# Kernel tuning notes

Measured on AMD Instinct MI355X. Metric: run time of the kernel, lower is better.

## Reference

```python
import jax, jax.numpy as jnp
import numpy as np

NH = 8          # attention heads
NC = 14         # disease classes
K = 10          # aspect queries per class
E = 1024        # vision_dim == text_dim
HID = 512       # hidden_dim = vision_dim // 2
TEMP = 0.1
LN_EPS = 1e-5


def _layernorm(x, g, b):
    m = jnp.mean(x, axis=-1, keepdims=True)
    v = jnp.mean(jnp.square(x - m), axis=-1, keepdims=True)
    return (x - m) * jax.lax.rsqrt(v + LN_EPS) * g + b


def _mha(q, k, v, in_w, in_b, out_w, out_b):
    # nn.MultiheadAttention (batch_first, eval mode => dropout off)
    B, Lq, Emb = q.shape
    Lk = k.shape[1]
    dh = Emb // NH
    wq, wk, wv = jnp.split(in_w, 3, axis=0)
    bq, bk, bv = jnp.split(in_b, 3)
    qh = (q @ wq.T + bq).reshape(B, Lq, NH, dh)
    kh = (k @ wk.T + bk).reshape(B, Lk, NH, dh)
    vh = (v @ wv.T + bv).reshape(B, Lk, NH, dh)
    scale = np.float32(1.0 / np.sqrt(dh))
    scores = jnp.einsum('bqhd,bkhd->bhqk', qh, kh) * scale
    attn = jax.nn.softmax(scores, axis=-1)
    out = jnp.einsum('bhqk,bkhd->bqhd', attn, vh).reshape(B, Lq, Emb)
    out = out @ out_w.T + out_b
    return out, attn.mean(axis=1)  # avg over heads, (B, Lq, Lk)


def _l2norm(x):
    return x / jnp.maximum(jnp.linalg.norm(x, axis=-1, keepdims=True), 1e-12)


def reference(vision_features, text_embeddings, vision_global, aspect_queries,
              ch_in_w, ch_in_b, ch_out_w, ch_out_b, tp_w, tp_b,
              ca_in_w, ca_in_b, ca_out_w, ca_out_b,
              cross_ln_g, cross_ln_b, cross_fc_w, cross_fc_b,
              dir_ln_g, dir_ln_b, dir_w1, dir_b1, dir_w2, dir_b2):
    B, N, _ = vision_features.shape
    # ---- contrastive branch (1-token query / 1-token kv attention) ----
    text_proj = text_embeddings @ tp_w.T + tp_b               # (B, E)
    c_out, _ = _mha(vision_global[:, None, :], text_proj[:, None, :],
                    text_proj[:, None, :], ch_in_w, ch_in_b, ch_out_w, ch_out_b)
    sim = jnp.sum(_l2norm(c_out[:, 0, :]) * _l2norm(text_proj), axis=-1) / TEMP  # (B,)
    contrastive_logits = jnp.broadcast_to(sim[:, None], (B, NC))
    # ---- supervised branch: fused per-class cross-attention (shared K/V) ----
    q = jnp.broadcast_to(aspect_queries.reshape(1, NC * K, E), (B, NC * K, E))
    att_out, attn_w = _mha(q, vision_features, vision_features,
                           ca_in_w, ca_in_b, ca_out_w, ca_out_b)
    attended = att_out.reshape(B, NC, K, E).mean(axis=2)       # (B, NC, E)
    attention_weights = attn_w.reshape(B, NC, K, N)            # (B, NC, K, N)
    # fc_cross: LN + per-class linear row (class j feature -> class j logit)
    h = _layernorm(attended, cross_ln_g, cross_ln_b)
    logits_cross = jnp.einsum('bjd,jd->bj', h, cross_fc_w) + cross_fc_b
    # fc_direct MLP on global feature
    g = _layernorm(vision_global, dir_ln_g, dir_ln_b)
    logits_direct = jax.nn.relu(g @ dir_w1.T + dir_b1) @ dir_w2.T + dir_b2
    supervised_logits = (logits_cross + logits_direct) * 0.5
    final_logits = (supervised_logits + contrastive_logits) * 0.5
    return contrastive_logits, supervised_logits, final_logits, attention_weights


def setup_inputs() -> dict:
    key = jax.random.key(0)
    ks = jax.random.split(key, 16)
    B, N = 64, 576
    w = lambda k, s: (jax.random.normal(k, s, dtype=jnp.float32) * 0.02)
    return {
        'vision_features': jax.random.normal(ks[0], (B, N, E), dtype=jnp.float32),
        'text_embeddings': jax.random.normal(ks[1], (B, E), dtype=jnp.float32),
        'vision_global': jax.random.normal(ks[2], (B, E), dtype=jnp.float32),
        'aspect_queries': jax.random.normal(ks[3], (NC, K, E), dtype=jnp.float32) / np.sqrt(E).astype(np.float32),
        'ch_in_w': w(ks[4], (3 * E, E)), 'ch_in_b': jnp.zeros((3 * E,), jnp.float32),
        'ch_out_w': w(ks[5], (E, E)), 'ch_out_b': jnp.zeros((E,), jnp.float32),
        'tp_w': w(ks[6], (E, E)), 'tp_b': jnp.zeros((E,), jnp.float32),
        'ca_in_w': w(ks[7], (3 * E, E)), 'ca_in_b': jnp.zeros((3 * E,), jnp.float32),
        'ca_out_w': w(ks[8], (E, E)), 'ca_out_b': jnp.zeros((E,), jnp.float32),
        'cross_ln_g': jnp.ones((E,), jnp.float32), 'cross_ln_b': jnp.zeros((E,), jnp.float32),
        'cross_fc_w': w(ks[9], (NC, E)), 'cross_fc_b': jnp.zeros((NC,), jnp.float32),
        'dir_ln_g': jnp.ones((E,), jnp.float32), 'dir_ln_b': jnp.zeros((E,), jnp.float32),
        'dir_w1': w(ks[10], (HID, E)), 'dir_b1': jnp.zeros((HID,), jnp.float32),
        'dir_w2': w(ks[11], (NC, HID)), 'dir_b2': jnp.zeros((NC,), jnp.float32),
    }
```

## Files before the change

kernel.cpp:

```cpp
#include <hip/hip_runtime.h>
#include <cstdio>
#include <cstdint>

using u16 = unsigned short;
typedef __bf16 bf16x8 __attribute__((ext_vector_type(8)));
typedef float f32x4 __attribute__((ext_vector_type(4)));

#define GLOBAL_AS __attribute__((address_space(1)))
#define LDS_AS __attribute__((address_space(3)))

__device__ __forceinline__ float bf2f(u16 h) {
  return __uint_as_float(((unsigned)h) << 16);
}
__device__ __forceinline__ u16 f2bf(float f) {
  unsigned u = __float_as_uint(f);
  u += 0x7FFFu + ((u >> 16) & 1u);
  return (u16)(u >> 16);
}

__device__ __forceinline__ void async_copy16(void* lds, const void* g) {
  __builtin_amdgcn_global_load_lds((const GLOBAL_AS unsigned int*)g,
                                   (LDS_AS unsigned int*)lds, 16, 0, 0);
}

__device__ __forceinline__ float block_sum(float v, float* red) {
#pragma unroll
  for (int o = 32; o >= 1; o >>= 1) v += __shfl_xor(v, o);
  __syncthreads();
  if ((threadIdx.x & 63) == 0) red[threadIdx.x >> 6] = v;
  __syncthreads();
  return red[0] + red[1] + red[2] + red[3];
}

__global__ __launch_bounds__(256) void cvt4_kernel(
    const float* __restrict__ s0, u16* __restrict__ d0,
    const float* __restrict__ s1, u16* __restrict__ d1,
    const float* __restrict__ s2, u16* __restrict__ d2,
    const float* __restrict__ s3, u16* __restrict__ d3) {
  const float* s; u16* d; long n; long b0; long nb;
  const int b = blockIdx.x;
  if (b < 2048)      { s = s0; d = d0; n = 37748736L; b0 = b;        nb = 2048; }
  else if (b < 2816) { s = s1; d = d1; n = 3145728L;  b0 = b - 2048; nb = 768; }
  else if (b < 3072) { s = s2; d = d2; n = 1048576L;  b0 = b - 2816; nb = 256; }
  else               { s = s3; d = d3; n = 143360L;   b0 = b - 3072; nb = 35; }
  long i = (b0 * 256 + threadIdx.x) * 4;
  const long stride = nb * 1024;
  for (; i < n; i += stride) {
    float4 v = *(const float4*)(s + i);
    ushort4 o;
    o.x = f2bf(v.x); o.y = f2bf(v.y); o.z = f2bf(v.z); o.w = f2bf(v.w);
    *(ushort4*)(d + i) = o;
  }
}

template <int VTD>
__global__ __launch_bounds__(512, 2) void gemm_kvq_kernel(
    const u16* __restrict__ A, const u16* __restrict__ Bkv,
    const u16* __restrict__ Aq, const u16* __restrict__ Bq,
    u16* __restrict__ Ck, u16* __restrict__ Cvp, u16* __restrict__ Vt,
    u16* __restrict__ Cq,
    const float* __restrict__ bias, const float* __restrict__ biasq) {
  __shared__ char smem[131072];
  const int bid = blockIdx.x;
  const int t = threadIdx.x;
  const int wid = t >> 6, l = t & 63;
  const int wm = wid >> 2, wn = wid & 3;
  const int lr = l & 15, lg = l >> 4, lr7 = lr & 7;

  int mt = 0, nt = 0, qb = -1;
  const u16* Abase; const u16* Bbase; const float* bias_b;
  if (bid < 1152) {
    const int wgid = (bid & 7) * 144 + (bid >> 3);
    mt = wgid >> 3; nt = wgid & 7;
    Abase = A + (size_t)mt * 256 * 1024;
    Bbase = Bkv + (size_t)nt * 256 * 1024;
    bias_b = bias + nt * 256;
  } else {
    qb = bid - 1152;
    Abase = Aq;
    Bbase = Bq + (size_t)qb * 256 * 1024;
    bias_b = biasq + qb * 256;
  }

  const int srow = t >> 3;
  const int scx = (t & 7) ^ (srow & 7);
  const char* Asrc = (const char*)Abase + (size_t)srow * 2048 + (scx << 4);
  const char* Bsrc = (const char*)Bbase + (size_t)srow * 2048 + (scx << 4);
  const int wb = wid << 10;

  f32x4 acc[8][4] = {};

#define SA(d, r, kt) async_copy16(smem + (d)*65536 + (r)*8192 + wb, \
                                  Asrc + (size_t)(r)*131072 + (size_t)(kt)*128)
#define SB(d, r, kt) async_copy16(smem + (d)*65536 + 32768 + (r)*8192 + wb, \
                                  Bsrc + (size_t)(r)*131072 + (size_t)(kt)*128)

#define RA(d, half)                                                          \
  _Pragma("unroll")                                                          \
  for (int i = 0; i < 4; ++i) {                                              \
    const int row = wm * 128 + ((half)*4 + i) * 16 + lr;                     \
    af[i][0] = *(const bf16x8*)(smem + (d)*65536 + (row << 7) + ((lg ^ lr7) << 4));       \
    af[i][1] = *(const bf16x8*)(smem + (d)*65536 + (row << 7) + (((4 | lg) ^ lr7) << 4)); \
  }

#define RB(d, half)                                                          \
  _Pragma("unroll")                                                          \
  for (int j = 0; j < 2; ++j) {                                              \
    const int row = wn * 64 + ((half)*2 + j) * 16 + lr;                      \
    bfr[j][0] = *(const bf16x8*)(smem + (d)*65536 + 32768 + (row << 7) + ((lg ^ lr7) << 4));       \
    bfr[j][1] = *(const bf16x8*)(smem + (d)*65536 + 32768 + (row << 7) + (((4 | lg) ^ lr7) << 4)); \
  }

#define MM(mh, nh)                                                           \
  __builtin_amdgcn_s_setprio(1);                                             \
  _Pragma("unroll")                                                          \
  for (int ks = 0; ks < 2; ++ks)                                             \
    _Pragma("unroll")                                                        \
    for (int i = 0; i < 4; ++i)                                              \
      _Pragma("unroll")                                                      \
      for (int j = 0; j < 2; ++j)                                            \
        acc[(mh)*4 + i][(nh)*2 + j] = __builtin_amdgcn_mfma_f32_16x16x32_bf16( \
            af[i][ks], bfr[j][ks], acc[(mh)*4 + i][(nh)*2 + j], 0, 0, 0);    \
  __builtin_amdgcn_s_setprio(0);

  SA(0, 0, 0); SA(0, 1, 0); SA(0, 2, 0); SA(0, 3, 0);
  SB(0, 0, 0); SB(0, 1, 0); SB(0, 2, 0); SB(0, 3, 0);
  SA(1, 0, 1); SA(1, 2, 1);
  asm volatile("s_waitcnt vmcnt(2)" ::: "memory");
  __builtin_amdgcn_s_barrier();
  asm volatile("" ::: "memory");

#pragma unroll 1
  for (int kt = 0; kt < 16; ++kt) {
    const int cur = kt & 1, nxt = cur ^ 1;
    const bool pf1 = (kt < 15), pf2 = (kt < 14);
    bf16x8 af[4][2], bfr[2][2];
    RA(cur, 0);
    RB(cur, 0);
    if (pf1) { SB(nxt, 0, kt + 1); SB(nxt, 1, kt + 1); }
    __builtin_amdgcn_s_barrier();
    asm volatile("s_waitcnt lgkmcnt(0)" ::: "memory");
    MM(0, 0);
    __builtin_amdgcn_s_barrier();
    RB(cur, 1);
    if (pf1) { SB(nxt, 2, kt + 1); SB(nxt, 3, kt + 1); }
    __builtin_amdgcn_s_barrier();
    asm volatile("s_waitcnt lgkmcnt(0)" ::: "memory");
    MM(0, 1);
    if (pf1) asm volatile("s_waitcnt vmcnt(6)" ::: "memory");
    __builtin_amdgcn_s_barrier();
    RA(cur, 1);
    if (pf1) { SA(nxt, 1, kt + 1); SA(nxt, 3, kt + 1); }
    __builtin_amdgcn_s_barrier();
    asm volatile("s_waitcnt lgkmcnt(0)" ::: "memory");
    MM(1, 1);
    __builtin_amdgcn_s_barrier();
    RB(cur, 0);
    if (pf2) { SA(cur, 0, kt + 2); SA(cur, 2, kt + 2); }
    __builtin_amdgcn_s_barrier();
    asm volatile("s_waitcnt lgkmcnt(0)" ::: "memory");
    MM(1, 0);
    if (pf2)      asm volatile("s_waitcnt vmcnt(4)" ::: "memory");
    else if (pf1) asm volatile("s_waitcnt vmcnt(0)" ::: "memory");
    __builtin_amdgcn_s_barrier();
  }
#undef SA
#undef SB
#undef RA
#undef RB
#undef MM

  if (VTD && qb < 0 && nt >= 4) {
    u16* T = (u16*)smem;
    const int vc2 = t >> 1, seg = t & 1;
    const int vglob = (nt - 4) * 256 + vc2;
    const int h2 = vglob >> 7, d2 = vglob & 127;
#pragma unroll 1
    for (int mh = 0; mh < 2; ++mh) {
      __syncthreads();
      if (wm == mh) {
#pragma unroll
        for (int ni = 0; ni < 4; ++ni) {
          const int vc = wn * 64 + ni * 16 + lr;
          const float bv = bias_b[vc];
#pragma unroll
          for (int mi = 0; mi < 8; ++mi) {
            const int ml = mi * 16 + lg * 4;
            ushort4 pk;
            pk.x = f2bf(acc[mi][ni][0] + bv);
            pk.y = f2bf(acc[mi][ni][1] + bv);
            pk.z = f2bf(acc[mi][ni][2] + bv);
            pk.w = f2bf(acc[mi][ni][3] + bv);
            *(ushort4*)(T + (size_t)vc * 136 + ml) = pk;
          }
        }
      }
      __syncthreads();
      const int mg0 = mt * 256 + mh * 128 + seg * 64;
      const int bb = (unsigned)mg0 / 576u;
      const int k0 = mg0 - bb * 576;
      u16* dst = Vt + ((size_t)(bb * 8 + h2) * 128 + d2) * 576 + k0;
      const u16* src = T + (size_t)vc2 * 136 + seg * 64;
#pragma unroll
      for (int i2 = 0; i2 < 8; ++i2)
        *(uint4*)(dst + i2 * 8) = *(const uint4*)(src + i2 * 8);
    }
  } else {
    u16* D; int cb0;
    if (qb >= 0)      { D = Cq;  cb0 = qb * 256; }
    else if (nt < 4)  { D = Ck;  cb0 = nt * 256; }
    else              { D = Cvp; cb0 = (nt - 4) * 256; }
#pragma unroll
    for (int ni = 0; ni < 4; ++ni) {
      const int nc = wn * 64 + ni * 16 + lr;
      const float bv = bias_b[nc];
      const int col = cb0 + nc;
#pragma unroll
      for (int mi = 0; mi < 8; ++mi) {
#pragma unroll
        for (int rg = 0; rg < 4; ++rg) {
          const size_t m = (size_t)mt * 256 + wm * 128 + mi * 16 + lg * 4 + rg;
          D[m * 1024 + col] = f2bf(acc[mi][ni][rg] + bv);
        }
      }
    }
  }
}

template <int OUTF32>
__global__ __launch_bounds__(512, 2) void gemm_big_kernel(
    const u16* __restrict__ A, const u16* __restrict__ B, void* __restrict__ Cv,
    const float* __restrict__ bias, float scale,
    int KT, int ntx, int Mlim, int Nlim,
    long lda, long ldb, long ldc, int bdiv,
    long sA0, long sA1, long sB0, long sB1, long sC0, long sC1) {
  __shared__ u16 lds[3][24576];
  const int bid = blockIdx.x;
  const int bh = blockIdx.y;
  const int bb0 = bh / bdiv, bb1 = bh % bdiv;
  const int mt = bid / ntx, nt = bid % ntx;
  const int t = threadIdx.x;
  const int wid = t >> 6, l = t & 63;
  const int wr = wid >> 1, wc = wid & 1;
  const int lr = l & 15, lg = l >> 4, lr7 = lr & 7;

  const long ldab = lda * 2, ldbb = ldb * 2;
  const u16* Abase = A + (long)bb0 * sA0 + (long)bb1 * sA1 + (long)mt * 256 * lda;
  const u16* Bbase = B + (long)bb0 * sB0 + (long)bb1 * sB1 + (long)nt * 128 * ldb;

  const int srow = t >> 3;
  const int scx = (t & 7) ^ (srow & 7);
  const char* Asrc = (const char*)Abase + (long)srow * ldab + (scx << 4);
  const char* Bsrc = (const char*)Bbase + (long)srow * ldbb + (scx << 4);
  const int wbA = wid << 10;

  char* b0 = (char*)lds[0];
  char* b1 = (char*)lds[1];
  char* b2 = (char*)lds[2];

  f32x4 acc[4][4] = {};

#define STAGE3G(dst, kt, part)                                              \
  {                                                                         \
    const long ko = (long)(kt) * 128;                                       \
    if ((part) == 0) {                                                      \
      async_copy16((dst) + wbA,          Asrc + ko);                        \
      async_copy16((dst) + 8192 + wbA,   Asrc + 64 * ldab + ko);            \
      async_copy16((dst) + 16384 + wbA,  Asrc + 128 * ldab + ko);           \
    } else {                                                                \
      async_copy16((dst) + 24576 + wbA,  Asrc + 192 * ldab + ko);           \
      async_copy16((dst) + 32768 + wbA,  Bsrc + ko);                        \
      async_copy16((dst) + 40960 + wbA,  Bsrc + 64 * ldbb + ko);            \
    }                                                                       \
  }

#define COMPUTE_KS(p, KS)                                                   \
  {                                                                         \
    const int ccol = (((KS) << 2) | lg) ^ lr7;                              \
    const char* pA = (p) + (((wr << 6) + lr) << 7) + (ccol << 4);           \
    const char* pB = (p) + 32768 + (((wc << 6) + lr) << 7) + (ccol << 4);   \
    bf16x8 af[4], bfr[4];                                                   \
    _Pragma("unroll")                                                       \
    for (int i = 0; i < 4; ++i) {                                           \
      af[i]  = *(const bf16x8*)(pA + i * 2048);                             \
      bfr[i] = *(const bf16x8*)(pB + i * 2048);                             \
    }                                                                       \
    __builtin_amdgcn_s_setprio(1);                                          \
    _Pragma("unroll")                                                       \
    for (int mi = 0; mi < 4; ++mi)                                          \
      _Pragma("unroll")                                                     \
      for (int ni = 0; ni < 4; ++ni)                                        \
        acc[mi][ni] = __builtin_amdgcn_mfma_f32_16x16x32_bf16(              \
            af[mi], bfr[ni], acc[mi][ni], 0, 0, 0);                         \
    __builtin_amdgcn_s_setprio(0);                                          \
  }

  STAGE3G(b0, 0, 0); STAGE3G(b0, 0, 1);
  STAGE3G(b1, 1, 0); STAGE3G(b1, 1, 1);
  asm volatile("s_waitcnt vmcnt(6)" ::: "memory");
  __builtin_amdgcn_s_barrier();
  asm volatile("" ::: "memory");

  char* p0 = b0; char* p1 = b1; char* p2 = b2;
#pragma unroll 1
  for (int kt = 0; kt < KT; ++kt) {
    const bool pf = (kt < KT - 2);
    if (pf) STAGE3G(p2, kt + 2, 0);
    COMPUTE_KS(p0, 0);
    if (pf) STAGE3G(p2, kt + 2, 1);
    COMPUTE_KS(p0, 1);
    if (kt < KT - 1) {
      if (pf) asm volatile("s_waitcnt vmcnt(6)" ::: "memory");
      else    asm volatile("s_waitcnt vmcnt(0)" ::: "memory");
      __builtin_amdgcn_s_barrier();
      asm volatile("" ::: "memory");
    }
    char* tmp = p0; p0 = p1; p1 = p2; p2 = tmp;
  }
#undef STAGE3G
#undef COMPUTE_KS

  const long cBase = (long)bb0 * sC0 + (long)bb1 * sC1;
  const int mr0 = mt * 256 + wr * 64 + lg * 4;
  const int nc0 = nt * 128 + wc * 64 + lr;
#pragma unroll
  for (int ni = 0; ni < 4; ++ni) {
    const int n = nc0 + ni * 16;
    if (n >= Nlim) continue;
    const float bv = bias ? bias[n] : 0.0f;
#pragma unroll
    for (int mi = 0; mi < 4; ++mi) {
#pragma unroll
      for (int rg = 0; rg < 4; ++rg) {
        const int m = mr0 + mi * 16 + rg;
        if (m >= Mlim) continue;
        const float v = acc[mi][ni][rg] * scale + bv;
        if (OUTF32) ((float*)Cv)[cBase + (long)m * ldc + n] = v;
        else        ((u16*)Cv)[cBase + (long)m * ldc + n] = f2bf(v);
      }
    }
  }
}

__global__ __launch_bounds__(256) void transpose_v_kernel(const u16* __restrict__ V,
                                                          u16* __restrict__ Vt) {
  __shared__ u16 tile[64][65];
  const int k0 = blockIdx.x * 64;
  const int c0 = blockIdx.y * 64;
  const int b = blockIdx.z;
  const int t = threadIdx.x;
  const int tx = t & 15, ty = t >> 4;
  const u16* Vb = V + (size_t)(b * 576) * 1024;
#pragma unroll
  for (int i = 0; i < 4; ++i) {
    const int k = ty + i * 16;
    const u16* src = Vb + (size_t)(k0 + k) * 1024 + c0 + tx * 4;
    ushort2 v01 = *(const ushort2*)src;
    ushort2 v23 = *(const ushort2*)(src + 2);
    tile[k][tx * 4 + 0] = v01.x; tile[k][tx * 4 + 1] = v01.y;
    tile[k][tx * 4 + 2] = v23.x; tile[k][tx * 4 + 3] = v23.y;
  }
  __syncthreads();
  const int h = c0 >> 7, d0 = c0 & 127;
  u16* VtB = Vt + ((size_t)(b * 8 + h) * 128 + d0) * 576 + k0;
#pragma unroll
  for (int i = 0; i < 4; ++i) {
    const int d = ty + i * 16;
    u16* dst = VtB + (size_t)d * 576 + tx * 4;
    ushort2 a, bb2;
    a.x = tile[tx * 4 + 0][d]; a.y = tile[tx * 4 + 1][d];
    bb2.x = tile[tx * 4 + 2][d]; bb2.y = tile[tx * 4 + 3][d];
    *(ushort2*)dst = a; *(ushort2*)(dst + 2) = bb2;
  }
}

__global__ __launch_bounds__(512) void softmax_pm_kernel(const u16* __restrict__ SP,
                                                         float* __restrict__ attnOut,
                                                         u16* __restrict__ Pm) {
  const int b = blockIdx.x, c = blockIdx.y;
  const int h = threadIdx.x >> 6, l = threadIdx.x & 63;
  __shared__ float pl[8][576];
  float pacc[9] = {};
#pragma unroll 1
  for (int qq = 0; qq < 10; ++qq) {
    const u16* row = SP + ((size_t)((b * 8 + h) * 144 + c * 10 + qq)) * 576;
    float x[9];
#pragma unroll
    for (int i = 0; i < 9; ++i) x[i] = bf2f(row[l + 64 * i]);
    float m = x[0];
#pragma unroll
    for (int i = 1; i < 9; ++i) m = fmaxf(m, x[i]);
#pragma unroll
    for (int o = 32; o >= 1; o >>= 1) m = fmaxf(m, __shfl_xor(m, o));
    float e[9], s = 0.f;
#pragma unroll
    for (int i = 0; i < 9; ++i) { e[i] = expf(x[i] - m); s += e[i]; }
#pragma unroll
    for (int o = 32; o >= 1; o >>= 1) s += __shfl_xor(s, o);
    const float inv = 1.f / s;
#pragma unroll
    for (int i = 0; i < 9; ++i) {
      const float p = e[i] * inv;
      pacc[i] += p;
      pl[h][l + 64 * i] = p;
    }
    __syncthreads();
    float* out = attnOut + ((size_t)(b * 140 + c * 10 + qq)) * 576;
    {
      const int j = threadIdx.x;
      float a = 0.f;
#pragma unroll
      for (int hh = 0; hh < 8; ++hh) a += pl[hh][j];
      out[j] = a * 0.125f;
      if (j < 64) {
        float a2 = 0.f;
#pragma unroll
        for (int hh = 0; hh < 8; ++hh) a2 += pl[hh][j + 512];
        out[j + 512] = a2 * 0.125f;
      }
    }
    __syncthreads();
  }
  u16* pm = Pm + ((size_t)((b * 8 + h) * 14 + c)) * 576;
#pragma unroll
  for (int i = 0; i < 9; ++i) pm[l + 64 * i] = f2bf(pacc[i] * 0.1f);
}

__global__ __launch_bounds__(256) void pv_small_kernel(const u16* __restrict__ Pm,
                                                       const u16* __restrict__ Vt,
                                                       u16* __restrict__ Attd) {
  const int b = blockIdx.x, h = blockIdx.y;
  const int t = threadIdx.x;
  const int w = t >> 6, l = t & 63;
  const int lr = l & 15, lg = l >> 4;
  __shared__ u16 pm[16][584];
  for (int i = t; i < 16 * 73; i += 256) {
    const int r = i / 73, ck = i - (i / 73) * 73;
    uint4 v = {0u, 0u, 0u, 0u};
    if (r < 14 && ck < 72)
      v = *(const uint4*)&Pm[((size_t)((b * 8 + h) * 14 + r)) * 576 + ck * 8];
    *(uint4*)&pm[r][ck * 8] = v;
  }
  __syncthreads();
  const u16* vbase = Vt + ((size_t)(b * 8 + h) * 128) * 576;
  f32x4 acc[2] = {};
#pragma unroll 1
  for (int ks = 0; ks < 18; ++ks) {
    const bf16x8 af = *(const bf16x8*)&pm[lr][ks * 32 + lg * 8];
#pragma unroll
    for (int j = 0; j < 2; ++j) {
      const int nf = w * 2 + j;
      const bf16x8 bf = *(const bf16x8*)&vbase[(size_t)(nf * 16 + lr) * 576 + ks * 32 + lg * 8];
      acc[j] = __builtin_amdgcn_mfma_f32_16x16x32_bf16(af, bf, acc[j], 0, 0, 0);
    }
  }
#pragma unroll
  for (int j = 0; j < 2; ++j) {
    const int nf = w * 2 + j;
#pragma unroll
    for (int rg = 0; rg < 4; ++rg) {
      const int cc = lg * 4 + rg;
      if (cc < 14)
        Attd[((size_t)b * 14 + cc) * 1024 + h * 128 + nf * 16 + lr] = f2bf(acc[j][rg]);
    }
  }
}

__global__ __launch_bounds__(256) void ln_crossfc_kernel(
    const float* __restrict__ ap, const float* __restrict__ g, const float* __restrict__ bb,
    const float* __restrict__ fw, const float* __restrict__ fb, float* __restrict__ out) {
  const int bc = blockIdx.x;
  const int c = bc % 14;
  const float* x = ap + (size_t)bc * 1024;
  __shared__ float red[4];
  const int t = threadIdx.x;
  float v[4];
  float s = 0.f;
#pragma unroll
  for (int i = 0; i < 4; ++i) { v[i] = x[t + i * 256]; s += v[i]; }
  const float mean = block_sum(s, red) * (1.f / 1024.f);
  float vs = 0.f;
#pragma unroll
  for (int i = 0; i < 4; ++i) { const float d = v[i] - mean; vs += d * d; }
  const float var = block_sum(vs, red) * (1.f / 1024.f);
  const float inv = rsqrtf(var + 1e-5f);
  float acc = 0.f;
#pragma unroll
  for (int i = 0; i < 4; ++i) {
    const int e = t + i * 256;
    const float h = (v[i] - mean) * inv * g[e] + bb[e];
    acc += h * fw[(size_t)c * 1024 + e];
  }
  acc = block_sum(acc, red);
  if (t == 0) out[bc] = acc + fb[c];
}

__global__ __launch_bounds__(256) void direct_mlp_kernel(
    const float* __restrict__ vg, const float* __restrict__ g, const float* __restrict__ bb,
    const float* __restrict__ w1, const float* __restrict__ b1,
    const float* __restrict__ w2, const float* __restrict__ b2, float* __restrict__ out) {
  const int b = blockIdx.x;
  __shared__ float red[4];
  __shared__ float gn[1024];
  __shared__ float h1[512];
  const int t = threadIdx.x;
  const float* x = vg + (size_t)b * 1024;
  float v[4];
  float s = 0.f;
#pragma unroll
  for (int i = 0; i < 4; ++i) { v[i] = x[t + i * 256]; s += v[i]; }
  const float mean = block_sum(s, red) * (1.f / 1024.f);
  float vs = 0.f;
#pragma unroll
  for (int i = 0; i < 4; ++i) { const float d = v[i] - mean; vs += d * d; }
  const float var = block_sum(vs, red) * (1.f / 1024.f);
  const float inv = rsqrtf(var + 1e-5f);
#pragma unroll
  for (int i = 0; i < 4; ++i) {
    const int e = t + i * 256;
    gn[e] = (v[i] - mean) * inv * g[e] + bb[e];
  }
  __syncthreads();
  for (int j = t; j < 512; j += 256) {
    float a = b1[j];
    const float4* wr = (const float4*)(w1 + (size_t)j * 1024);
    const float4* g4 = (const float4*)gn;
    for (int e = 0; e < 256; ++e) {
      float4 wv = wr[e], av = g4[e];
      a += av.x * wv.x + av.y * wv.y + av.z * wv.z + av.w * wv.w;
    }
    h1[j] = fmaxf(a, 0.f);
  }
  __syncthreads();
  for (int c = 0; c < 14; ++c) {
    float a = 0.f;
    for (int j = t; j < 512; j += 256) a += h1[j] * w2[(size_t)c * 512 + j];
    a = block_sum(a, red);
    if (t == 0) out[b * 14 + c] = a + b2[c];
  }
}

__global__ __launch_bounds__(256) void linear_f32_kernel(
    const float* __restrict__ A, const float* __restrict__ W, const float* __restrict__ bias,
    float* __restrict__ C, int N, int Kd) {
  const int r = blockIdx.x;
  const int j = blockIdx.y * 256 + threadIdx.x;
  __shared__ float a[1024];
  for (int e = threadIdx.x; e < Kd; e += 256) a[e] = A[(size_t)r * Kd + e];
  __syncthreads();
  float acc = bias ? bias[j] : 0.f;
  const float4* wr = (const float4*)(W + (size_t)j * Kd);
  const float4* a4 = (const float4*)a;
  for (int e = 0; e < Kd / 4; ++e) {
    float4 wv = wr[e], av = a4[e];
    acc += av.x * wv.x + av.y * wv.y + av.z * wv.z + av.w * wv.w;
  }
  C[(size_t)r * N + j] = acc;
}

__global__ __launch_bounds__(256) void sim_combine_kernel(
    const float* __restrict__ co, const float* __restrict__ tp,
    const float* __restrict__ lc, const float* __restrict__ ld,
    float* __restrict__ out) {
  const int b = blockIdx.x;
  const int t = threadIdx.x;
  __shared__ float red[4];
  const float* c = co + (size_t)b * 1024;
  const float* p = tp + (size_t)b * 1024;
  float dd = 0.f, nc = 0.f, nt = 0.f;
  for (int e = t; e < 1024; e += 256) {
    const float cv = c[e], pv = p[e];
    dd += cv * pv; nc += cv * cv; nt += pv * pv;
  }
  dd = block_sum(dd, red);
  nc = block_sum(nc, red);
  nt = block_sum(nt, red);
  const float sim = dd / (fmaxf(sqrtf(nc), 1e-12f) * fmaxf(sqrtf(nt), 1e-12f)) / 0.1f;
  if (t < 14) {
    const int i = b * 14 + t;
    const float sup = 0.5f * (lc[i] + ld[i]);
    out[i] = sim;
    out[896 + i] = sup;
    out[1792 + i] = 0.5f * (sup + sim);
  }
}

static constexpr size_t OFF_X    = 0;
static constexpr size_t OFF_K    = OFF_X + 75497472;
static constexpr size_t OFF_SP   = OFF_K + 75759616;
static constexpr size_t OFF_WIN  = OFF_SP + 85082112;
static constexpr size_t OFF_WOUT = OFF_WIN + 6291456;
static constexpr size_t OFF_ASP  = OFF_WOUT + 2097152;
static constexpr size_t OFF_QASP = OFF_ASP + 524288;
static constexpr size_t OFF_ATT  = OFF_QASP + 524288;
static constexpr size_t OFF_APRJ = OFF_ATT + 1835008;
static constexpr size_t OFF_TP   = OFF_APRJ + 3670016;
static constexpr size_t OFF_CV   = OFF_TP + 262144;
static constexpr size_t OFF_CO   = OFF_CV + 262144;
static constexpr size_t OFF_SIM  = OFF_CO + 262144;
static constexpr size_t OFF_LC   = OFF_SIM + 4096;
static constexpr size_t OFF_LD   = OFF_LC + 4096;
static constexpr size_t WS_SMALL = OFF_LD + 4096;
static constexpr size_t OFF_VT   = WS_SMALL;
static constexpr size_t WS_BIG   = OFF_VT + 75497472;

extern "C" void kernel_launch(void* const* d_in, const int* in_sizes, int n_in,
                              void* d_out, int out_size, void* d_ws, size_t ws_size,
                              hipStream_t stream) {
  (void)in_sizes; (void)n_in; (void)out_size;
  const float* vision_features = (const float*)d_in[0];
  const float* text_embeddings = (const float*)d_in[1];
  const float* vision_global   = (const float*)d_in[2];
  const float* aspect_queries  = (const float*)d_in[3];
  const float* ch_in_w  = (const float*)d_in[4];
  const float* ch_in_b  = (const float*)d_in[5];
  const float* ch_out_w = (const float*)d_in[6];
  const float* ch_out_b = (const float*)d_in[7];
  const float* tp_w = (const float*)d_in[8];
  const float* tp_b = (const float*)d_in[9];
  const float* ca_in_w  = (const float*)d_in[10];
  const float* ca_in_b  = (const float*)d_in[11];
  const float* ca_out_w = (const float*)d_in[12];
  const float* ca_out_b = (const float*)d_in[13];
  const float* cross_ln_g = (const float*)d_in[14];
  const float* cross_ln_b = (const float*)d_in[15];
  const float* cross_fc_w = (const float*)d_in[16];
  const float* cross_fc_b = (const float*)d_in[17];
  const float* dir_ln_g = (const float*)d_in[18];
  const float* dir_ln_b = (const float*)d_in[19];
  const float* dir_w1 = (const float*)d_in[20];
  const float* dir_b1 = (const float*)d_in[21];
  const float* dir_w2 = (const float*)d_in[22];
  const float* dir_b2 = (const float*)d_in[23];

  if (ws_size < WS_SMALL) {
    fprintf(stderr, "kernel_launch: ws too small: %zu < %zu\n", ws_size, WS_SMALL);
    return;
  }
  const bool big = (ws_size >= WS_BIG);

  char* ws = (char*)d_ws;
  u16* Xb      = (u16*)(ws + OFF_X);
  u16* Kb      = (u16*)(ws + OFF_K);
  u16* Pm      = (u16*)(ws + OFF_K);
  u16* Vb      = (u16*)(ws + OFF_SP);
  u16* SP      = (u16*)(ws + OFF_SP);
  u16* Vt      = big ? (u16*)(ws + OFF_VT) : (u16*)(ws + OFF_X);
  u16* Win     = (u16*)(ws + OFF_WIN);
  u16* Wout    = (u16*)(ws + OFF_WOUT);
  u16* Asp     = (u16*)(ws + OFF_ASP);
  u16* Qasp    = (u16*)(ws + OFF_QASP);
  u16* Attd    = (u16*)(ws + OFF_ATT);
  float* Aprj  = (float*)(ws + OFF_APRJ);
  float* Tp    = (float*)(ws + OFF_TP);
  float* Cv2   = (float*)(ws + OFF_CV);
  float* Co    = (float*)(ws + OFF_CO);
  float* Lc    = (float*)(ws + OFF_LC);
  float* Ld    = (float*)(ws + OFF_LD);
  float* attnOut = (float*)d_out + 2688;

  cvt4_kernel<<<3107, 256, 0, stream>>>(vision_features, Xb, ca_in_w, Win,
                                        ca_out_w, Wout, aspect_queries, Asp);

  if (big) {
    gemm_kvq_kernel<1><<<dim3(1156), 512, 0, stream>>>(
        Xb, Win + 1024 * 1024, Asp, Win, Kb, nullptr, Vt, Qasp,
        ca_in_b + 1024, ca_in_b);
  } else {
    gemm_kvq_kernel<0><<<dim3(1156), 512, 0, stream>>>(
        Xb, Win + 1024 * 1024, Asp, Win, Kb, Vb, nullptr, Qasp,
        ca_in_b + 1024, ca_in_b);
    transpose_v_kernel<<<dim3(9, 16, 64), 256, 0, stream>>>(Vb, Vt);
  }

  gemm_big_kernel<0><<<dim3(5, 512), 512, 0, stream>>>(
      Qasp, Kb, SP, nullptr, 0.08838834764831845f,
      2, 5, 140, 576, 1024, 1024, 576, 8,
      0L, 128L, 589824L, 128L, 663552L, 82944L);

  softmax_pm_kernel<<<dim3(64, 14), 512, 0, stream>>>(SP, attnOut, Pm);

  pv_small_kernel<<<dim3(64, 8), 256, 0, stream>>>(Pm, Vt, Attd);

  gemm_big_kernel<1><<<dim3(32, 1), 512, 0, stream>>>(
      Attd, Wout, Aprj, ca_out_b, 1.0f,
      16, 8, 896, 1024, 1024, 1024, 1024, 1,
      0L, 0L, 0L, 0L, 0L, 0L);

  ln_crossfc_kernel<<<896, 256, 0, stream>>>(Aprj, cross_ln_g, cross_ln_b,
                                             cross_fc_w, cross_fc_b, Lc);

  direct_mlp_kernel<<<64, 256, 0, stream>>>(vision_global, dir_ln_g, dir_ln_b,
                                            dir_w1, dir_b1, dir_w2, dir_b2, Ld);

  linear_f32_kernel<<<dim3(64, 4), 256, 0, stream>>>(text_embeddings, tp_w, tp_b, Tp, 1024, 1024);
  linear_f32_kernel<<<dim3(64, 4), 256, 0, stream>>>(Tp, ch_in_w + 2048 * 1024, ch_in_b + 2048, Cv2, 1024, 1024);
  linear_f32_kernel<<<dim3(64, 4), 256, 0, stream>>>(Cv2, ch_out_w, ch_out_b, Co, 1024, 1024);

  sim_combine_kernel<<<64, 256, 0, stream>>>(Co, Tp, Lc, Ld, (float*)d_out);
}
```

Before: 598.1 us.

## Piggyback small contrastive/MLP branch kernels onto existing big kernels' grids

Removes the standalone direct_mlp and three linear_f32 launches and folds them as extra blocks into the cvt, score GEMM, and softmax kernels. The dependency chain Tp -> Cv2 -> Co is kept by placing each stage in a successive kernel. This cuts launch count and lets the small fp32 matvec work overlap with the large kernels' tails. The cost is extra registers and LDS pressure in the host kernels, plus extra blocks that can steal CUs from the main work.

Result: slower. 672.2 us (+12.4%).

```diff
diff --git a/kernel.cpp b/kernel.cpp
--- a/kernel.cpp
+++ b/kernel.cpp
@@ -32,24 +32,93 @@
   return red[0] + red[1] + red[2] + red[3];
 }
 
-__global__ __launch_bounds__(256) void cvt4_kernel(
+__global__ __launch_bounds__(256) void cvt4p_kernel(
     const float* __restrict__ s0, u16* __restrict__ d0,
     const float* __restrict__ s1, u16* __restrict__ d1,
     const float* __restrict__ s2, u16* __restrict__ d2,
-    const float* __restrict__ s3, u16* __restrict__ d3) {
-  const float* s; u16* d; long n; long b0; long nb;
+    const float* __restrict__ s3, u16* __restrict__ d3,
+    const float* __restrict__ te, const float* __restrict__ tpw,
+    const float* __restrict__ tpb, float* __restrict__ Tp,
+    const float* __restrict__ vg, const float* __restrict__ g,
+    const float* __restrict__ bb,
+    const float* __restrict__ w1, const float* __restrict__ b1,
+    const float* __restrict__ w2, const float* __restrict__ b2,
+    float* __restrict__ Ld) {
+  __shared__ float sbuf[1540];
   const int b = blockIdx.x;
-  if (b < 2048)      { s = s0; d = d0; n = 37748736L; b0 = b;        nb = 2048; }
-  else if (b < 2816) { s = s1; d = d1; n = 3145728L;  b0 = b - 2048; nb = 768; }
-  else if (b < 3072) { s = s2; d = d2; n = 1048576L;  b0 = b - 2816; nb = 256; }
-  else               { s = s3; d = d3; n = 143360L;   b0 = b - 3072; nb = 35; }
-  long i = (b0 * 256 + threadIdx.x) * 4;
-  const long stride = nb * 1024;
-  for (; i < n; i += stride) {
-    float4 v = *(const float4*)(s + i);
-    ushort4 o;
-    o.x = f2bf(v.x); o.y = f2bf(v.y); o.z = f2bf(v.z); o.w = f2bf(v.w);
-    *(ushort4*)(d + i) = o;
+  const int t = threadIdx.x;
+  if (b < 3107) {
+    const float* s; u16* d; long n; long b0; long nb;
+    if (b < 2048)      { s = s0; d = d0; n = 37748736L; b0 = b;        nb = 2048; }
+    else if (b < 2816) { s = s1; d = d1; n = 3145728L;  b0 = b - 2048; nb = 768; }
+    else if (b < 3072) { s = s2; d = d2; n = 1048576L;  b0 = b - 2816; nb = 256; }
+    else               { s = s3; d = d3; n = 143360L;   b0 = b - 3072; nb = 35; }
+    long i = (b0 * 256 + t) * 4;
+    const long stride = nb * 1024;
+    for (; i < n; i += stride) {
+      float4 v = *(const float4*)(s + i);
+      ushort4 o;
+      o.x = f2bf(v.x); o.y = f2bf(v.y); o.z = f2bf(v.z); o.w = f2bf(v.w);
+      *(ushort4*)(d + i) = o;
+    }
+    return;
+  }
+  if (b < 3363) {
+    const int blk = b - 3107;
+    const int r = blk >> 2, jb = blk & 3;
+    float* a = sbuf;
+    for (int e = t; e < 1024; e += 256) a[e] = te[(size_t)r * 1024 + e];
+    __syncthreads();
+    const int j = jb * 256 + t;
+    float acc = tpb[j];
+    const float4* wr = (const float4*)(tpw + (size_t)j * 1024);
+    const float4* a4 = (const float4*)a;
+    for (int e = 0; e < 256; ++e) {
+      float4 wv = wr[e], av = a4[e];
+      acc += av.x * wv.x + av.y * wv.y + av.z * wv.z + av.w * wv.w;
+    }
+    Tp[(size_t)r * 1024 + j] = acc;
+    return;
+  }
+  {
+    const int bm = b - 3363;
+    float* gn = sbuf;
+    float* h1 = sbuf + 1024;
+    float* red = sbuf + 1536;
+    const float* x = vg + (size_t)bm * 1024;
+    float v[4];
+    float s = 0.f;
+#pragma unroll
+    for (int i = 0; i < 4; ++i) { v[i] = x[t + i * 256]; s += v[i]; }
+    const float mean = block_sum(s, red) * (1.f / 1024.f);
+    float vs = 0.f;
+#pragma unroll
+    for (int i = 0; i < 4; ++i) { const float d = v[i] - mean; vs += d * d; }
+    const float var = block_sum(vs, red) * (1.f / 1024.f);
+    const float inv = rsqrtf(var + 1e-5f);
+#pragma unroll
+    for (int i = 0; i < 4; ++i) {
+      const int e = t + i * 256;
+      gn[e] = (v[i] - mean) * inv * g[e] + bb[e];
+    }
+    __syncthreads();
+    for (int j = t; j < 512; j += 256) {
+      float a = b1[j];
+      const float4* wr = (const float4*)(w1 + (size_t)j * 1024);
+      const float4* g4 = (const float4*)gn;
+      for (int e = 0; e < 256; ++e) {
+        float4 wv = wr[e], av = g4[e];
+        a += av.x * wv.x + av.y * wv.y + av.z * wv.z + av.w * wv.w;
+      }
+      h1[j] = fmaxf(a, 0.f);
+    }
+    __syncthreads();
+    for (int c = 0; c < 14; ++c) {
+      float a = 0.f;
+      for (int j = t; j < 512; j += 256) a += h1[j] * w2[(size_t)c * 512 + j];
+      a = block_sum(a, red);
+      if (t == 0) Ld[bm * 14 + c] = a + b2[c];
+    }
   }
 }
 
@@ -227,19 +296,43 @@
   }
 }
 
-template <int OUTF32>
+template <int OUTF32, int PACK>
 __global__ __launch_bounds__(512, 2) void gemm_big_kernel(
     const u16* __restrict__ A, const u16* __restrict__ B, void* __restrict__ Cv,
     const float* __restrict__ bias, float scale,
     int KT, int ntx, int Mlim, int Nlim,
     long lda, long ldb, long ldc, int bdiv,
-    long sA0, long sA1, long sB0, long sB1, long sC0, long sC1) {
+    long sA0, long sA1, long sB0, long sB1, long sC0, long sC1,
+    const float* __restrict__ pA, const float* __restrict__ pW,
+    const float* __restrict__ pBias, float* __restrict__ pC) {
   __shared__ u16 lds[3][24576];
   const int bid = blockIdx.x;
   const int bh = blockIdx.y;
+  const int t = threadIdx.x;
+
+  if (PACK && bid >= ntx * ((Mlim + 255) / 256)) {
+    if (bh < 256) {
+      const int r = bh >> 2, jb = bh & 3;
+      float* a = (float*)lds;
+      for (int e = t; e < 1024; e += 512) a[e] = pA[(size_t)r * 1024 + e];
+      __syncthreads();
+      if (t < 256) {
+        const int j = jb * 256 + t;
+        float acc = pBias[j];
+        const float4* wr = (const float4*)(pW + (size_t)j * 1024);
+        const float4* a4 = (const float4*)a;
+        for (int e = 0; e < 256; ++e) {
+          float4 wv = wr[e], av = a4[e];
+          acc += av.x * wv.x + av.y * wv.y + av.z * wv.z + av.w * wv.w;
+        }
+        pC[(size_t)r * 1024 + j] = acc;
+      }
+    }
+    return;
+  }
+
   const int bb0 = bh / bdiv, bb1 = bh % bdiv;
   const int mt = bid / ntx, nt = bid % ntx;
-  const int t = threadIdx.x;
   const int wid = t >> 6, l = t & 63;
   const int wr = wid >> 1, wc = wid & 1;
   const int lr = l & 15, lg = l >> 4, lr7 = lr & 7;
@@ -277,13 +370,13 @@
 #define COMPUTE_KS(p, KS)                                                   \
   {                                                                         \
     const int ccol = (((KS) << 2) | lg) ^ lr7;                              \
-    const char* pA = (p) + (((wr << 6) + lr) << 7) + (ccol << 4);           \
-    const char* pB = (p) + 32768 + (((wc << 6) + lr) << 7) + (ccol << 4);   \
+    const char* pAx = (p) + (((wr << 6) + lr) << 7) + (ccol << 4);          \
+    const char* pBx = (p) + 32768 + (((wc << 6) + lr) << 7) + (ccol << 4);  \
     bf16x8 af[4], bfr[4];                                                   \
     _Pragma("unroll")                                                       \
     for (int i = 0; i < 4; ++i) {                                           \
-      af[i]  = *(const bf16x8*)(pA + i * 2048);                             \
-      bfr[i] = *(const bf16x8*)(pB + i * 2048);                             \
+      af[i]  = *(const bf16x8*)(pAx + i * 2048);                            \
+      bfr[i] = *(const bf16x8*)(pBx + i * 2048);                            \
     }                                                                       \
     __builtin_amdgcn_s_setprio(1);                                          \
     _Pragma("unroll")                                                       \
@@ -374,12 +467,32 @@
   }
 }
 
-__global__ __launch_bounds__(512) void softmax_pm_kernel(const u16* __restrict__ SP,
-                                                         float* __restrict__ attnOut,
-                                                         u16* __restrict__ Pm) {
+__global__ __launch_bounds__(512) void softmax_pm_kernel(
+    const u16* __restrict__ SP, float* __restrict__ attnOut, u16* __restrict__ Pm,
+    const float* __restrict__ Cv2, const float* __restrict__ Wco,
+    const float* __restrict__ bco, float* __restrict__ Co) {
+  __shared__ float pl[8][576];
+  if (blockIdx.y >= 14) {
+    const int r = blockIdx.x, jb = blockIdx.y - 14;
+    const int t = threadIdx.x;
+    float* a = (float*)pl;
+    for (int e = t; e < 1024; e += 512) a[e] = Cv2[(size_t)r * 1024 + e];
+    __syncthreads();
+    if (t < 256) {
+      const int j = jb * 256 + t;
+      float acc = bco[j];
+      const float4* wr = (const float4*)(Wco + (size_t)j * 1024);
+      const float4* a4 = (const float4*)a;
+      for (int e = 0; e < 256; ++e) {
+        float4 wv = wr[e], av = a4[e];
+        acc += av.x * wv.x + av.y * wv.y + av.z * wv.z + av.w * wv.w;
+      }
+      Co[(size_t)r * 1024 + j] = acc;
+    }
+    return;
+  }
   const int b = blockIdx.x, c = blockIdx.y;
   const int h = threadIdx.x >> 6, l = threadIdx.x & 63;
-  __shared__ float pl[8][576];
   float pacc[9] = {};
 #pragma unroll 1
   for (int qq = 0; qq < 10; ++qq) {
@@ -493,69 +606,6 @@
   }
   acc = block_sum(acc, red);
   if (t == 0) out[bc] = acc + fb[c];
-}
-
-__global__ __launch_bounds__(256) void direct_mlp_kernel(
-    const float* __restrict__ vg, const float* __restrict__ g, const float* __restrict__ bb,
-    const float* __restrict__ w1, const float* __restrict__ b1,
-    const float* __restrict__ w2, const float* __restrict__ b2, float* __restrict__ out) {
-  const int b = blockIdx.x;
-  __shared__ float red[4];
-  __shared__ float gn[1024];
-  __shared__ float h1[512];
-  const int t = threadIdx.x;
-  const float* x = vg + (size_t)b * 1024;
-  float v[4];
-  float s = 0.f;
-#pragma unroll
-  for (int i = 0; i < 4; ++i) { v[i] = x[t + i * 256]; s += v[i]; }
-  const float mean = block_sum(s, red) * (1.f / 1024.f);
-  float vs = 0.f;
-#pragma unroll
-  for (int i = 0; i < 4; ++i) { const float d = v[i] - mean; vs += d * d; }
-  const float var = block_sum(vs, red) * (1.f / 1024.f);
-  const float inv = rsqrtf(var + 1e-5f);
-#pragma unroll
-  for (int i = 0; i < 4; ++i) {
-    const int e = t + i * 256;
-    gn[e] = (v[i] - mean) * inv * g[e] + bb[e];
-  }
-  __syncthreads();
-  for (int j = t; j < 512; j += 256) {
-    float a = b1[j];
-    const float4* wr = (const float4*)(w1 + (size_t)j * 1024);
-    const float4* g4 = (const float4*)gn;
-    for (int e = 0; e < 256; ++e) {
-      float4 wv = wr[e], av = g4[e];
-      a += av.x * wv.x + av.y * wv.y + av.z * wv.z + av.w * wv.w;
-    }
-    h1[j] = fmaxf(a, 0.f);
-  }
-  __syncthreads();
-  for (int c = 0; c < 14; ++c) {
-    float a = 0.f;
-    for (int j = t; j < 512; j += 256) a += h1[j] * w2[(size_t)c * 512 + j];
-    a = block_sum(a, red);
-    if (t == 0) out[b * 14 + c] = a + b2[c];
-  }
-}
-
-__global__ __launch_bounds__(256) void linear_f32_kernel(
-    const float* __restrict__ A, const float* __restrict__ W, const float* __restrict__ bias,
-    float* __restrict__ C, int N, int Kd) {
-  const int r = blockIdx.x;
-  const int j = blockIdx.y * 256 + threadIdx.x;
-  __shared__ float a[1024];
-  for (int e = threadIdx.x; e < Kd; e += 256) a[e] = A[(size_t)r * Kd + e];
-  __syncthreads();
-  float acc = bias ? bias[j] : 0.f;
-  const float4* wr = (const float4*)(W + (size_t)j * Kd);
-  const float4* a4 = (const float4*)a;
-  for (int e = 0; e < Kd / 4; ++e) {
-    float4 wv = wr[e], av = a4[e];
-    acc += av.x * wv.x + av.y * wv.y + av.z * wv.z + av.w * wv.w;
-  }
-  C[(size_t)r * N + j] = acc;
 }
 
 __global__ __launch_bounds__(256) void sim_combine_kernel(
@@ -659,8 +709,10 @@
   float* Ld    = (float*)(ws + OFF_LD);
   float* attnOut = (float*)d_out + 2688;
 
-  cvt4_kernel<<<3107, 256, 0, stream>>>(vision_features, Xb, ca_in_w, Win,
-                                        ca_out_w, Wout, aspect_queries, Asp);
+  cvt4p_kernel<<<3427, 256, 0, stream>>>(
+      vision_features, Xb, ca_in_w, Win, ca_out_w, Wout, aspect_queries, Asp,
+      text_embeddings, tp_w, tp_b, Tp,
+      vision_global, dir_ln_g, dir_ln_b, dir_w1, dir_b1, dir_w2, dir_b2, Ld);
 
   if (big) {
     gemm_kvq_kernel<1><<<dim3(1156), 512, 0, stream>>>(
@@ -673,29 +725,25 @@
     transpose_v_kernel<<<dim3(9, 16, 64), 256, 0, stream>>>(Vb, Vt);
   }
 
-  gemm_big_kernel<0><<<dim3(5, 512), 512, 0, stream>>>(
+  gemm_big_kernel<0, 1><<<dim3(6, 512), 512, 0, stream>>>(
       Qasp, Kb, SP, nullptr, 0.08838834764831845f,
       2, 5, 140, 576, 1024, 1024, 576, 8,
-      0L, 128L, 589824L, 128L, 663552L, 82944L);
-
-  softmax_pm_kernel<<<dim3(64, 14), 512, 0, stream>>>(SP, attnOut, Pm);
+      0L, 128L, 589824L, 128L, 663552L, 82944L,
+      Tp, ch_in_w + 2048 * 1024, ch_in_b + 2048, Cv2);
+
+  softmax_pm_kernel<<<dim3(64, 18), 512, 0, stream>>>(
+      SP, attnOut, Pm, Cv2, ch_out_w, ch_out_b, Co);
 
   pv_small_kernel<<<dim3(64, 8), 256, 0, stream>>>(Pm, Vt, Attd);
 
-  gemm_big_kernel<1><<<dim3(32, 1), 512, 0, stream>>>(
+  gemm_big_kernel<1, 0><<<dim3(32, 1), 512, 0, stream>>>(
       Attd, Wout, Aprj, ca_out_b, 1.0f,
       16, 8, 896, 1024, 1024, 1024, 1024, 1,
-      0L, 0L, 0L, 0L, 0L, 0L);
+      0L, 0L, 0L, 0L, 0L, 0L,
+      nullptr, nullptr, nullptr, nullptr);
 
   ln_crossfc_kernel<<<896, 256, 0, stream>>>(Aprj, cross_ln_g, cross_ln_b,
                                              cross_fc_w, cross_fc_b, Lc);
 
-  direct_mlp_kernel<<<64, 256, 0, stream>>>(vision_global, dir_ln_g, dir_ln_b,
-                                            dir_w1, dir_b1, dir_w2, dir_b2, Ld);
-
-  linear_f32_kernel<<<dim3(64, 4), 256, 0, stream>>>(text_embeddings, tp_w, tp_b, Tp, 1024, 1024);
-  linear_f32_kernel<<<dim3(64, 4), 256, 0, stream>>>(Tp, ch_in_w + 2048 * 1024, ch_in_b + 2048, Cv2, 1024, 1024);
-  linear_f32_kernel<<<dim3(64, 4), 256, 0, stream>>>(Cv2, ch_out_w, ch_out_b, Co, 1024, 1024);
-
   sim_combine_kernel<<<64, 256, 0, stream>>>(Co, Tp, Lc, Ld, (float*)d_out);
 }
```
